# Kernel optimization log

Hardware: AMD Instinct MI355X
Metric: run time of the kernel (lower is better)

## Reference

```python
import jax, jax.numpy as jnp
import numpy as np

N_NODES = 100000
N_EDGES = 3200000
IN_CH = 256
HID = 256   # 2 * out_channels
OUT = 128


def _gcn_norm(edge_index, n):
    # PyG GCNConv normalization: add self-loops, norm = d^-1/2[src] * d^-1/2[dst]
    src, dst = edge_index[0], edge_index[1]
    loops = jnp.arange(n, dtype=src.dtype)
    src = jnp.concatenate([src, loops])
    dst = jnp.concatenate([dst, loops])
    ones = jnp.ones_like(dst, dtype=jnp.float32)
    deg = jax.ops.segment_sum(ones, dst, num_segments=n)
    dinv = jnp.where(deg > 0, jax.lax.rsqrt(deg), 0.0)
    norm = dinv[src] * dinv[dst]
    return src, dst, norm


def _gcn_conv(x, W, b, src, dst, norm, n):
    h = x @ W                              # [N, F_out] dense transform first (F_out <= F_in)
    msg = h[src] * norm[:, None]           # gather + scale  [E+N, F_out]
    out = jax.ops.segment_sum(msg, dst, num_segments=n)  # scatter-add
    return out + b


def setup_inputs() -> dict:
    key = jax.random.key(0)
    k1, k2, k3, k4 = jax.random.split(key, 4)
    x = jax.random.normal(k1, (N_NODES, IN_CH), dtype=jnp.float32)
    edge_index = jax.random.randint(k2, (2, N_EDGES), 0, N_NODES, dtype=jnp.int64)
    # Glorot-style init for weights, zero bias (PyG GCNConv defaults)
    W1 = jax.random.normal(k3, (IN_CH, HID), dtype=jnp.float32) * (1.0 / np.sqrt(IN_CH))
    b1 = jnp.zeros((HID,), dtype=jnp.float32)
    W2 = jax.random.normal(k4, (HID, OUT), dtype=jnp.float32) * (1.0 / np.sqrt(HID))
    b2 = jnp.zeros((OUT,), dtype=jnp.float32)
    return {"x": x, "edge_index": edge_index, "W1": W1, "b1": b1, "W2": W2, "b2": b2}


def reference(x, edge_index, W1, b1, W2, b2):
    n = x.shape[0]
    src, dst, norm = _gcn_norm(edge_index, n)  # cached=True: shared across both layers
    h = _gcn_conv(x, W1, b1, src, dst, norm, n)
    h = jax.nn.relu(h)
    z = _gcn_conv(h, W2, b2, src, dst, norm, n)
    return z
```

## Files before the change

### kernel.cpp

```cpp
#include <hip/hip_runtime.h>
#include <cstdio>


#define NPB 256
#define PCHUNK 8192

template <int V> struct vec_t;
template <> struct vec_t<2> {
  typedef float    fv __attribute__((ext_vector_type(2)));
  typedef _Float16 hv __attribute__((ext_vector_type(2)));
};
template <> struct vec_t<4> {
  typedef float    fv __attribute__((ext_vector_type(4)));
  typedef _Float16 hv __attribute__((ext_vector_type(4)));
};

__global__ __launch_bounds__(256) void k_zero(int* p, int n) {
  int i = blockIdx.x * 256 + threadIdx.x;
  if (i < n) p[i] = 0;
}

__global__ __launch_bounds__(256) void k_bhist(const int* __restrict__ dst,
                                               int* __restrict__ bcnt,
                                               int e, int nb) {
  __shared__ int h[512];
  for (int i = threadIdx.x; i < nb; i += 256) h[i] = 0;
  __syncthreads();
  int c0 = blockIdx.x * PCHUNK;
  int c1 = min(c0 + PCHUNK, e);
  for (int i = c0 + threadIdx.x; i < c1; i += 256)
    atomicAdd(&h[dst[i] >> 8], 1);
  __syncthreads();
  for (int i = threadIdx.x; i < nb; i += 256)
    if (h[i]) atomicAdd(&bcnt[i], h[i]);
}

__global__ __launch_bounds__(512) void k_bscan(const int* __restrict__ bcnt,
                                               int* __restrict__ bbase,
                                               int* __restrict__ gcur, int nb) {
  __shared__ int sm[512];
  int tid = threadIdx.x;
  sm[tid] = (tid < nb) ? bcnt[tid] : 0;
  __syncthreads();
  for (int d = 1; d < 512; d <<= 1) {
    int t = (tid >= d) ? sm[tid - d] : 0;
    __syncthreads();
    sm[tid] += t;
    __syncthreads();
  }
  int ex = (tid == 0) ? 0 : sm[tid - 1];
  if (tid < nb) {
    bbase[tid] = ex;
    gcur[tid] = ex;
  }
  if (tid == nb) bbase[nb] = sm[nb - 1];
}

__global__ __launch_bounds__(256) void k_partition(const int* __restrict__ src,
                                                   const int* __restrict__ dst,
                                                   int* __restrict__ gcur,
                                                   uint2* __restrict__ tmp,
                                                   int e, int nb) {
  __shared__ int hist[512];
  __shared__ int base[512];
  for (int i = threadIdx.x; i < nb; i += 256) hist[i] = 0;
  __syncthreads();
  int c0 = blockIdx.x * PCHUNK;
  int c1 = min(c0 + PCHUNK, e);
  for (int i = c0 + threadIdx.x; i < c1; i += 256)
    atomicAdd(&hist[dst[i] >> 8], 1);
  __syncthreads();
  for (int i = threadIdx.x; i < nb; i += 256) {
    int c = hist[i];
    base[i] = c ? atomicAdd(&gcur[i], c) : 0;
    hist[i] = 0;
  }
  __syncthreads();
  for (int i = c0 + threadIdx.x; i < c1; i += 256) {
    int d = dst[i];
    int b = d >> 8;
    int pos = base[b] + atomicAdd(&hist[b], 1);
    uint2 v;
    v.x = (unsigned)src[i];
    v.y = (unsigned)d;
    tmp[pos] = v;
  }
}

__global__ __launch_bounds__(256) void k_bucket(const uint2* __restrict__ tmp,
                                                const int* __restrict__ bbase,
                                                int* __restrict__ off,
                                                float* __restrict__ dinv,
                                                int* __restrict__ esrc, int n) {
  __shared__ int lcnt[NPB];
  __shared__ int lsum[NPB];
  __shared__ int lcur[NPB];
  const int b = blockIdx.x;
  const int tid = threadIdx.x;
  const int r0 = b << 8;
  const int nn = min(NPB, n - r0);
  const int lo = bbase[b], hi = bbase[b + 1];

  lcnt[tid] = 0;
  __syncthreads();
  for (int i = lo + tid; i < hi; i += 256)
    atomicAdd(&lcnt[tmp[i].y & (NPB - 1)], 1);
  __syncthreads();
  lsum[tid] = lcnt[tid];
  __syncthreads();
  for (int d = 1; d < NPB; d <<= 1) {
    int t = (tid >= d) ? lsum[tid - d] : 0;
    __syncthreads();
    lsum[tid] += t;
    __syncthreads();
  }
  int ex = (tid == 0) ? 0 : lsum[tid - 1];
  if (tid < nn) {
    off[r0 + tid] = lo + ex;
    dinv[r0 + tid] = rsqrtf((float)(lcnt[tid] + 1));
    lcur[tid] = lo + ex;
  }
  if (r0 + nn == n && tid == 0) off[n] = hi;
  __syncthreads();
  for (int i = lo + tid; i < hi; i += 256) {
    uint2 t2 = tmp[i];
    int pos = atomicAdd(&lcur[t2.y & (NPB - 1)], 1);
    esrc[pos] = (int)t2.x;
  }
}

template <typename AT>
__global__ __launch_bounds__(256) void k_gemm(const AT* __restrict__ A,
                                              const float* __restrict__ B,
                                              _Float16* __restrict__ C,
                                              int M, int N, int K) {
  __shared__ __align__(16) float As[16][68];
  __shared__ __align__(16) float Bs[16][64];
  const int tid = threadIdx.x;
  const int bm = blockIdx.x * 64;
  const int bn = blockIdx.y * 64;
  const int tx = tid & 15, ty = tid >> 4;

  const int arow = tid >> 2;
  const int akk  = (tid & 3) * 4;
  const int brow = tid >> 4;
  const int bcol = (tid & 15) * 4;
  const bool avalid = (bm + arow) < M;

  float acc[4][4] = {};

  for (int k0 = 0; k0 < K; k0 += 16) {
    float4 av = make_float4(0.f, 0.f, 0.f, 0.f);
    if (avalid) {
      const AT* ap = A + (size_t)(bm + arow) * K + k0 + akk;
      if constexpr (sizeof(AT) == 4) {
        av = *(const float4*)ap;
      } else {
        vec_t<4>::hv t = *(const vec_t<4>::hv*)ap;
        av = make_float4((float)t.x, (float)t.y, (float)t.z, (float)t.w);
      }
    }
    float4 bv = *(const float4*)(B + (size_t)(k0 + brow) * N + bn + bcol);
    __syncthreads();
    As[akk + 0][arow] = av.x;
    As[akk + 1][arow] = av.y;
    As[akk + 2][arow] = av.z;
    As[akk + 3][arow] = av.w;
    *(float4*)&Bs[brow][bcol] = bv;
    __syncthreads();
#pragma unroll
    for (int k = 0; k < 16; ++k) {
      float4 a = *(const float4*)&As[k][ty * 4];
      float4 b = *(const float4*)&Bs[k][tx * 4];
      float ar[4] = {a.x, a.y, a.z, a.w};
      float br[4] = {b.x, b.y, b.z, b.w};
#pragma unroll
      for (int ii = 0; ii < 4; ++ii)
#pragma unroll
        for (int jj = 0; jj < 4; ++jj)
          acc[ii][jj] += ar[ii] * br[jj];
    }
  }

#pragma unroll
  for (int ii = 0; ii < 4; ++ii) {
    int row = bm + ty * 4 + ii;
    if (row < M) {
      vec_t<4>::hv v;
      v.x = (_Float16)acc[ii][0];
      v.y = (_Float16)acc[ii][1];
      v.z = (_Float16)acc[ii][2];
      v.w = (_Float16)acc[ii][3];
      *(vec_t<4>::hv*)&C[(size_t)row * N + bn + tx * 4] = v;
    }
  }
}

template <int C, bool RELU, typename OutT>
__global__ __launch_bounds__(256) void k_agg(const _Float16* __restrict__ h,
                                             const int* __restrict__ esrc,
                                             const int* __restrict__ off,
                                             const float* __restrict__ dinv,
                                             const float* __restrict__ bias,
                                             OutT* __restrict__ out, int n) {
  constexpr int V = C / 64;
  typedef typename vec_t<V>::fv FV;
  typedef typename vec_t<V>::hv HV;
  int gwave = (blockIdx.x * 256 + threadIdx.x) >> 6;
  int lane = threadIdx.x & 63;
  if (gwave >= n) return;
  const int i = gwave;
  const float di = dinv[i];

  FV acc = di * __builtin_convertvector(
                    *(const HV*)(h + (size_t)i * C + lane * V), FV);

  int e = off[i];
  const int e1 = off[i + 1];
  for (; e + 3 < e1; e += 4) {
    int s0 = esrc[e], s1 = esrc[e + 1], s2 = esrc[e + 2], s3 = esrc[e + 3];
    float w0 = dinv[s0], w1 = dinv[s1], w2 = dinv[s2], w3 = dinv[s3];
    HV v0 = *(const HV*)(h + (size_t)s0 * C + lane * V);
    HV v1 = *(const HV*)(h + (size_t)s1 * C + lane * V);
    HV v2 = *(const HV*)(h + (size_t)s2 * C + lane * V);
    HV v3 = *(const HV*)(h + (size_t)s3 * C + lane * V);
    acc += w0 * __builtin_convertvector(v0, FV);
    acc += w1 * __builtin_convertvector(v1, FV);
    acc += w2 * __builtin_convertvector(v2, FV);
    acc += w3 * __builtin_convertvector(v3, FV);
  }
  for (; e < e1; ++e) {
    int s = esrc[e];
    acc += dinv[s] * __builtin_convertvector(
                         *(const HV*)(h + (size_t)s * C + lane * V), FV);
  }

  FV bv = *(const FV*)(bias + lane * V);
  FV r = acc * di + bv;
  if (RELU) {
#pragma unroll
    for (int v = 0; v < V; ++v) r[v] = fmaxf(r[v], 0.f);
  }
  if constexpr (sizeof(OutT) == 2) {
    *(HV*)(out + (size_t)i * C + lane * V) = __builtin_convertvector(r, HV);
  } else {
    *(FV*)(out + (size_t)i * C + lane * V) = r;
  }
}

extern "C" void kernel_launch(void* const* d_in, const int* in_sizes, int n_in,
                              void* d_out, int out_size, void* d_ws, size_t ws_size,
                              hipStream_t stream) {
  const float* x  = (const float*)d_in[0];
  const int*   ei = (const int*)d_in[1];
  const float* W1 = (const float*)d_in[2];
  const float* b1 = (const float*)d_in[3];
  const float* W2 = (const float*)d_in[4];
  const float* b2 = (const float*)d_in[5];
  float* out = (float*)d_out;

  const int IN_CH = 256, HID = 256, OUT = 128;
  const int N = in_sizes[0] / IN_CH;
  const int E = in_sizes[1] / 2;
  const int* src = ei;
  const int* dst = ei + E;
  const int NB = (N + NPB - 1) / NPB;

  char* p = (char*)d_ws;
  auto alloc = [&](size_t bytes) {
    void* r = (void*)p;
    p += (bytes + 255) & ~(size_t)255;
    return r;
  };
  _Float16* h1   = (_Float16*)alloc((size_t)N * HID * 2);
  _Float16* h1r  = (_Float16*)alloc((size_t)N * HID * 2);
  int*      esrc = (int*)alloc((size_t)E * 4);
  uint2*    tmp  = (uint2*)alloc((size_t)E * 8);
  int*      off  = (int*)alloc((size_t)(N + 1) * 4);
  float*    dinv = (float*)alloc((size_t)N * 4);
  int*      bcnt = (int*)alloc((size_t)(NB + 1) * 4);
  int*      bbase= (int*)alloc((size_t)(NB + 1) * 4);
  int*      gcur = (int*)alloc((size_t)(NB + 1) * 4);
  if ((size_t)(p - (char*)d_ws) > ws_size) {
    fprintf(stderr, "kernel_launch: ws too small (need %zu, have %zu)\n",
            (size_t)(p - (char*)d_ws), ws_size);
    return;
  }

  const int nBlkP = (E + PCHUNK - 1) / PCHUNK;

  k_zero<<<(NB + 255) / 256, 256, 0, stream>>>(bcnt, NB);
  k_bhist<<<nBlkP, 256, 0, stream>>>(dst, bcnt, E, NB);
  k_bscan<<<1, 512, 0, stream>>>(bcnt, bbase, gcur, NB);
  k_partition<<<nBlkP, 256, 0, stream>>>(src, dst, gcur, tmp, E, NB);
  k_bucket<<<NB, 256, 0, stream>>>(tmp, bbase, off, dinv, esrc, N);
  dim3 g1((N + 63) / 64, HID / 64);
  k_gemm<float><<<g1, 256, 0, stream>>>(x, W1, h1, N, HID, IN_CH);
  int aggBlk = (N + 3) / 4;
  k_agg<256, true, _Float16><<<aggBlk, 256, 0, stream>>>(h1, esrc, off, dinv, b1, h1r, N);
  dim3 g2((N + 63) / 64, OUT / 64);
  k_gemm<_Float16><<<g2, 256, 0, stream>>>(h1r, W2, h1, N, OUT, HID);
  k_agg<128, false, float><<<aggBlk, 256, 0, stream>>>(h1, esrc, off, dinv, b2, out, N);
}
```

Baseline: 883.8 us.

## Replace FP32 SIMT GEMMs with split-FP16 MFMA GEMMs

Replaces the scalar FP32 shared-memory GEMM with a 128x128-tile MFMA kernel using 16x16x32 f16 instructions. To keep accuracy close to FP32, weights are split into high and low FP16 parts (pre-transposed by a new cast kernel), and for the first layer the FP32 input is split on the fly as well, giving three MFMA terms. The aim is to move the dense transforms onto matrix cores and cut the GEMM share of total time. The cost is extra MFMA work per term, small cast kernels, B fragments read directly from global memory rather than shared memory, and slightly different rounding.

```diff
diff --git a/kernel.cpp b/kernel.cpp
--- a/kernel.cpp
+++ b/kernel.cpp
@@ -14,6 +14,9 @@
   typedef float    fv __attribute__((ext_vector_type(4)));
   typedef _Float16 hv __attribute__((ext_vector_type(4)));
 };
+typedef _Float16 half4v __attribute__((ext_vector_type(4)));
+typedef _Float16 half8v __attribute__((ext_vector_type(8)));
+typedef float    f32x4  __attribute__((ext_vector_type(4)));
 
 __global__ __launch_bounds__(256) void k_zero(int* p, int n) {
   int i = blockIdx.x * 256 + threadIdx.x;
@@ -129,71 +132,114 @@
   }
 }
 
-template <typename AT>
-__global__ __launch_bounds__(256) void k_gemm(const AT* __restrict__ A,
-                                              const float* __restrict__ B,
-                                              _Float16* __restrict__ C,
-                                              int M, int N, int K) {
-  __shared__ __align__(16) float As[16][68];
-  __shared__ __align__(16) float Bs[16][64];
+__global__ __launch_bounds__(256) void k_castWT(const float* __restrict__ W,
+                                                _Float16* __restrict__ WhT,
+                                                _Float16* __restrict__ WlT,
+                                                int K, int N) {
+  int i = blockIdx.x * 256 + threadIdx.x;
+  if (i >= K * N) return;
+  int n = i % N, k = i / N;
+  float v = W[i];
+  _Float16 h = (_Float16)v;
+  WhT[(size_t)n * K + k] = h;
+  WlT[(size_t)n * K + k] = (_Float16)(v - (float)h);
+}
+
+template <typename AT, int NTERMS>
+__global__ __launch_bounds__(256, 2) void k_gemm_mfma(
+    const AT* __restrict__ A, const _Float16* __restrict__ BhT,
+    const _Float16* __restrict__ BlT, _Float16* __restrict__ C,
+    int M, int N, int K) {
+  constexpr bool SPLITA = (NTERMS == 3);
+  __shared__ _Float16 Ah[128][40];
+  __shared__ _Float16 Al[SPLITA ? 128 : 1][40];
+
   const int tid = threadIdx.x;
-  const int bm = blockIdx.x * 64;
-  const int bn = blockIdx.y * 64;
-  const int tx = tid & 15, ty = tid >> 4;
-
-  const int arow = tid >> 2;
-  const int akk  = (tid & 3) * 4;
-  const int brow = tid >> 4;
-  const int bcol = (tid & 15) * 4;
+  const int bm = blockIdx.x * 128;
+  const int bn = blockIdx.y * 128;
+
+  const int arow = tid >> 1;
+  const int acol = (tid & 1) * 16;
   const bool avalid = (bm + arow) < M;
-
-  float acc[4][4] = {};
-
-  for (int k0 = 0; k0 < K; k0 += 16) {
-    float4 av = make_float4(0.f, 0.f, 0.f, 0.f);
+  const AT* aptr = A + (size_t)(bm + arow) * K + acol;
+
+  const int wave = tid >> 6, lane = tid & 63;
+  const int wm = (wave & 1) * 64, wn = (wave >> 1) * 64;
+  const int lr = lane & 15, quad = lane >> 4;
+
+  const _Float16* bh0 = BhT + (size_t)(bn + wn + lr) * K + quad * 8;
+  const _Float16* bl0 = BlT + (size_t)(bn + wn + lr) * K + quad * 8;
+
+  f32x4 acc[4][4] = {};
+
+  for (int k0 = 0; k0 < K; k0 += 32) {
+    __syncthreads();
     if (avalid) {
-      const AT* ap = A + (size_t)(bm + arow) * K + k0 + akk;
-      if constexpr (sizeof(AT) == 4) {
-        av = *(const float4*)ap;
-      } else {
-        vec_t<4>::hv t = *(const vec_t<4>::hv*)ap;
-        av = make_float4((float)t.x, (float)t.y, (float)t.z, (float)t.w);
+#pragma unroll
+      for (int ii = 0; ii < 4; ++ii) {
+        if constexpr (SPLITA) {
+          f32x4 v = *(const f32x4*)(aptr + k0 + ii * 4);
+          half4v hv, lv;
+#pragma unroll
+          for (int j = 0; j < 4; ++j) {
+            hv[j] = (_Float16)v[j];
+            lv[j] = (_Float16)(v[j] - (float)hv[j]);
+          }
+          *(half4v*)&Ah[arow][acol + ii * 4] = hv;
+          *(half4v*)&Al[arow][acol + ii * 4] = lv;
+        } else {
+          half4v v = *(const half4v*)(aptr + k0 + ii * 4);
+          *(half4v*)&Ah[arow][acol + ii * 4] = v;
+        }
+      }
+    } else {
+      half4v z = {};
+#pragma unroll
+      for (int ii = 0; ii < 4; ++ii) {
+        *(half4v*)&Ah[arow][acol + ii * 4] = z;
+        if constexpr (SPLITA) *(half4v*)&Al[arow][acol + ii * 4] = z;
       }
     }
-    float4 bv = *(const float4*)(B + (size_t)(k0 + brow) * N + bn + bcol);
-    __syncthreads();
-    As[akk + 0][arow] = av.x;
-    As[akk + 1][arow] = av.y;
-    As[akk + 2][arow] = av.z;
-    As[akk + 3][arow] = av.w;
-    *(float4*)&Bs[brow][bcol] = bv;
-    __syncthreads();
-#pragma unroll
-    for (int k = 0; k < 16; ++k) {
-      float4 a = *(const float4*)&As[k][ty * 4];
-      float4 b = *(const float4*)&Bs[k][tx * 4];
-      float ar[4] = {a.x, a.y, a.z, a.w};
-      float br[4] = {b.x, b.y, b.z, b.w};
-#pragma unroll
-      for (int ii = 0; ii < 4; ++ii)
-#pragma unroll
-        for (int jj = 0; jj < 4; ++jj)
-          acc[ii][jj] += ar[ii] * br[jj];
+    __syncthreads();
+
+    half8v af[4], alf[4], bhf[4], blf[4];
+#pragma unroll
+    for (int mi = 0; mi < 4; ++mi) {
+      af[mi] = *(const half8v*)&Ah[wm + mi * 16 + lr][quad * 8];
+      if constexpr (SPLITA)
+        alf[mi] = *(const half8v*)&Al[wm + mi * 16 + lr][quad * 8];
     }
-  }
-
-#pragma unroll
-  for (int ii = 0; ii < 4; ++ii) {
-    int row = bm + ty * 4 + ii;
-    if (row < M) {
-      vec_t<4>::hv v;
-      v.x = (_Float16)acc[ii][0];
-      v.y = (_Float16)acc[ii][1];
-      v.z = (_Float16)acc[ii][2];
-      v.w = (_Float16)acc[ii][3];
-      *(vec_t<4>::hv*)&C[(size_t)row * N + bn + tx * 4] = v;
+#pragma unroll
+    for (int ni = 0; ni < 4; ++ni) {
+      bhf[ni] = *(const half8v*)(bh0 + (size_t)(ni * 16) * K + k0);
+      blf[ni] = *(const half8v*)(bl0 + (size_t)(ni * 16) * K + k0);
     }
-  }
+#pragma unroll
+    for (int mi = 0; mi < 4; ++mi)
+#pragma unroll
+      for (int ni = 0; ni < 4; ++ni) {
+        acc[mi][ni] = __builtin_amdgcn_mfma_f32_16x16x32_f16(
+            af[mi], bhf[ni], acc[mi][ni], 0, 0, 0);
+        acc[mi][ni] = __builtin_amdgcn_mfma_f32_16x16x32_f16(
+            af[mi], blf[ni], acc[mi][ni], 0, 0, 0);
+        if constexpr (SPLITA)
+          acc[mi][ni] = __builtin_amdgcn_mfma_f32_16x16x32_f16(
+              alf[mi], bhf[ni], acc[mi][ni], 0, 0, 0);
+      }
+  }
+
+#pragma unroll
+  for (int mi = 0; mi < 4; ++mi)
+#pragma unroll
+    for (int r = 0; r < 4; ++r) {
+      int row = bm + wm + mi * 16 + quad * 4 + r;
+      if (row < M) {
+#pragma unroll
+        for (int ni = 0; ni < 4; ++ni)
+          C[(size_t)row * N + bn + wn + ni * 16 + lr] =
+              (_Float16)acc[mi][ni][r];
+      }
+    }
 }
 
 template <int C, bool RELU, typename OutT>
@@ -281,6 +327,10 @@
   int*      bcnt = (int*)alloc((size_t)(NB + 1) * 4);
   int*      bbase= (int*)alloc((size_t)(NB + 1) * 4);
   int*      gcur = (int*)alloc((size_t)(NB + 1) * 4);
+  _Float16* w1h  = (_Float16*)alloc((size_t)IN_CH * HID * 2);
+  _Float16* w1l  = (_Float16*)alloc((size_t)IN_CH * HID * 2);
+  _Float16* w2h  = (_Float16*)alloc((size_t)HID * OUT * 2);
+  _Float16* w2l  = (_Float16*)alloc((size_t)HID * OUT * 2);
   if ((size_t)(p - (char*)d_ws) > ws_size) {
     fprintf(stderr, "kernel_launch: ws too small (need %zu, have %zu)\n",
             (size_t)(p - (char*)d_ws), ws_size);
@@ -294,11 +344,13 @@
   k_bscan<<<1, 512, 0, stream>>>(bcnt, bbase, gcur, NB);
   k_partition<<<nBlkP, 256, 0, stream>>>(src, dst, gcur, tmp, E, NB);
   k_bucket<<<NB, 256, 0, stream>>>(tmp, bbase, off, dinv, esrc, N);
-  dim3 g1((N + 63) / 64, HID / 64);
-  k_gemm<float><<<g1, 256, 0, stream>>>(x, W1, h1, N, HID, IN_CH);
+  k_castWT<<<(IN_CH * HID + 255) / 256, 256, 0, stream>>>(W1, w1h, w1l, IN_CH, HID);
+  k_castWT<<<(HID * OUT + 255) / 256, 256, 0, stream>>>(W2, w2h, w2l, HID, OUT);
+  dim3 g1((N + 127) / 128, HID / 128);
+  k_gemm_mfma<float, 3><<<g1, 256, 0, stream>>>(x, w1h, w1l, h1, N, HID, IN_CH);
   int aggBlk = (N + 3) / 4;
   k_agg<256, true, _Float16><<<aggBlk, 256, 0, stream>>>(h1, esrc, off, dinv, b1, h1r, N);
-  dim3 g2((N + 63) / 64, OUT / 64);
-  k_gemm<_Float16><<<g2, 256, 0, stream>>>(h1r, W2, h1, N, OUT, HID);
+  dim3 g2((N + 127) / 128, OUT / 128);
+  k_gemm_mfma<_Float16, 2><<<g2, 256, 0, stream>>>(h1r, w2h, w2l, h1, N, OUT, HID);
   k_agg<128, false, float><<<aggBlk, 256, 0, stream>>>(h1, esrc, off, dinv, b2, out, N);
 }
```

After: 746.9 us. 15.5% less time.
